# Kernel tuning notes

Hardware: AMD Instinct MI355X
Metric: run time of the kernel (lower is better)

The kernel has to match this reference:

```python
import jax, jax.numpy as jnp
import numpy as np

B, S, IN, H, K, V, OUT = 16, 200, 128, 128, 10, 50000, 10000
TW, DW = 1.0, 1.0  # time_window, dist_window


def setup_inputs() -> dict:
    key = jax.random.key(0)
    ks = jax.random.split(key, 12)
    full_seq = jax.random.randint(ks[0], (B, S), 0, V)
    length = jax.random.randint(ks[1], (B,), 1, S + 1)
    timestamp = jnp.sort(jax.random.uniform(ks[2], (B, S)), axis=1)  # sorted -> causal time_delta >= 0
    lat = jax.random.uniform(ks[3], (B, S))
    lng = jax.random.uniform(ks[4], (B, S))
    embed_table = jax.random.normal(ks[5], (V, IN)) * 0.05
    time_weights = jax.random.normal(ks[6], (K + 1, IN, H)) * (1.0 / np.sqrt(IN))
    dist_weights = jax.random.normal(ks[7], (K + 1, IN, H)) * (1.0 / np.sqrt(IN))
    hidden_weights = jax.random.normal(ks[8], (H, H)) * (1.0 / np.sqrt(H))
    W1 = jax.random.normal(ks[9], (H, 4 * H)) * 0.05
    b1 = jnp.zeros((4 * H,))
    W2 = jax.random.normal(ks[10], (4 * H, OUT)) * 0.05
    b2 = jnp.zeros((OUT,))
    return dict(full_seq=full_seq, length=length, timestamp=timestamp, lat=lat, lng=lng,
                embed_table=embed_table, time_weights=time_weights, dist_weights=dist_weights,
                hidden_weights=hidden_weights, W1=W1, b1=b1, W2=W2, b2=b2)


def reference(full_seq, length, timestamp, lat, lng, embed_table, time_weights,
              dist_weights, hidden_weights, W1, b1, W2, b2):
    x = embed_table[full_seq]                                   # [B,S,IN] (embed_layer)
    # pairwise time delta and context mask (valid target + causal j<=i + time window)
    td = timestamp[:, :, None] - timestamp[:, None, :]          # [B,S(i),S(j)]
    valid_j = length[:, None] > jnp.arange(S)[None, :]          # [B,S(j)]
    tri = jnp.arange(S)[:, None] >= jnp.arange(S)[None, :]      # i >= j (per-step slicing)
    mask = (td <= TW) & (td >= 0) & valid_j[:, None, :] & tri[None]
    # pairwise euclidean distance on (lat,lng)
    latlng = jnp.stack([lat, lng], axis=-1)                     # [B,S,2]
    dist = jnp.sqrt(((latlng[:, :, None] - latlng[:, None]) ** 2).sum(-1))
    t_idx = jnp.floor(jnp.clip(td, 0.0, TW) / TW * K).astype(jnp.int32)    # [B,S,S] in [0,K]
    d_idx = jnp.floor(jnp.clip(dist, 0.0, DW) / DW * K).astype(jnp.int32)
    # project each token x[b,j] through every slot's weight once, then gather per (i,j) bucket
    # (identical math to gathering W[t_idx] then x @ W, but avoids [B,S,S,IN,H])
    proj_t = jnp.einsum('bji,kio->bjko', x, time_weights)       # [B,S,K+1,H]
    proj_d = jnp.einsum('bji,kio->bjko', x, dist_weights)
    bI = jnp.arange(B)[:, None, None]
    jI = jnp.arange(S)[None, None, :]
    cand = 0.5 * proj_d[bI, jI, d_idx] + 0.5 * proj_t[bI, jI, t_idx]       # [B,S,S,H]
    X = jnp.where(mask[..., None], cand, 0.0).sum(2)            # [B,S,H] masked sum over context j
    # sequential sigmoid recurrence: h_i = sigmoid(X_i + h_{i-1} @ Wh)
    def step(h, xt):
        h = jax.nn.sigmoid(xt + h @ hidden_weights)
        return h, h
    _, outs = jax.lax.scan(step, jnp.zeros((B, H), X.dtype), X.transpose(1, 0, 2))
    rnn_out = outs.transpose(1, 0, 2)                           # [B,S,H]
    h_pre = rnn_out[jnp.arange(B), length - 1]                  # [B,H]
    # out_linear (dropout in eval mode = identity)
    return jnp.tanh(h_pre @ W1 + b1) @ W2 + b2                  # [B,OUT]
```

## Files before the change

kernel.cpp:

```cpp
#include <hip/hip_runtime.h>
#include <hip/hip_bf16.h>
#include <math.h>

#define B 16
#define S 200
#define IN 128
#define H 128
#define NK 11
#define OUTN 10000
#define H4 512

__global__ __launch_bounds__(512) void k_proj(
        const int* __restrict__ seq, const float* __restrict__ table,
        const int* __restrict__ length,
        const float* __restrict__ tw, const float* __restrict__ dw,
        float* __restrict__ pt, float* __restrict__ pd) {
    __shared__ float xs[32][68];
    __shared__ float wsm[32][128];
    __shared__ int sneed;
    int tid = threadIdx.x;
    int r0blk = blockIdx.x * 64;
    if (tid == 0) sneed = 0;
    __syncthreads();
    if (tid < 64) {
        int r = r0blk + tid;
        int bb = r / S, ii = r - bb * S;
        if (ii < length[bb]) sneed = 1;
    }
    __syncthreads();
    if (!sneed) return;

    int which = blockIdx.y / NK;
    int kb = blockIdx.y % NK;
    const float* W = (which == 0 ? tw : dw) + kb * IN * H;
    float* P = (which == 0 ? pt : pd);
    int tr = tid >> 5;
    int tc = tid & 31;
    int rr0 = tr * 4;

    float acc[4][4] = {{0.f}};
    for (int kk = 0; kk < IN; kk += 32) {
        {
            int r = tid >> 3;
            int kq = (tid & 7) * 4;
            int sv = seq[r0blk + r];
            float4 v = *reinterpret_cast<const float4*>(&table[sv * IN + kk + kq]);
            xs[kq + 0][r] = v.x; xs[kq + 1][r] = v.y;
            xs[kq + 2][r] = v.z; xs[kq + 3][r] = v.w;
        }
        #pragma unroll
        for (int i = 0; i < 2; ++i) {
            int f = tid + i * 512;
            int k = f >> 5; int c4 = f & 31;
            *reinterpret_cast<float4*>(&wsm[k][c4 * 4]) =
                *reinterpret_cast<const float4*>(&W[(kk + k) * H + c4 * 4]);
        }
        __syncthreads();
        #pragma unroll
        for (int k = 0; k < 32; ++k) {
            float4 a = *reinterpret_cast<const float4*>(&xs[k][rr0]);
            float4 w = *reinterpret_cast<const float4*>(&wsm[k][tc * 4]);
            acc[0][0] += a.x * w.x; acc[0][1] += a.x * w.y; acc[0][2] += a.x * w.z; acc[0][3] += a.x * w.w;
            acc[1][0] += a.y * w.x; acc[1][1] += a.y * w.y; acc[1][2] += a.y * w.z; acc[1][3] += a.y * w.w;
            acc[2][0] += a.z * w.x; acc[2][1] += a.z * w.y; acc[2][2] += a.z * w.z; acc[2][3] += a.z * w.w;
            acc[3][0] += a.w * w.x; acc[3][1] += a.w * w.y; acc[3][2] += a.w * w.z; acc[3][3] += a.w * w.w;
        }
        __syncthreads();
    }
    #pragma unroll
    for (int i = 0; i < 4; ++i) {
        int r = r0blk + rr0 + i;
        float4 v = make_float4(acc[i][0], acc[i][1], acc[i][2], acc[i][3]);
        *reinterpret_cast<float4*>(&P[(r * NK + kb) * H + tc * 4]) = v;
    }
}

__global__ __launch_bounds__(512) void k_xsum(const float* __restrict__ pt, const float* __restrict__ pd,
                       const int* __restrict__ length, const float* __restrict__ ts,
                       const float* __restrict__ lat, const float* __restrict__ lng,
                       float* __restrict__ X) {
    int wg = blockIdx.x;
    int idx = wg >> 3;
    int b = (wg & 7) + 8 * (idx / S);
    int i = idx % S;
    int len = length[b];
    if (i >= len) return;
    __shared__ float sts[S], sla[S], sln[S];
    __shared__ float psum[16][128];
    int tid = threadIdx.x;
    int jg = tid >> 5, c = tid & 31;
    if (tid < S) {
        sts[tid] = ts[b * S + tid]; sla[tid] = lat[b * S + tid]; sln[tid] = lng[b * S + tid];
    }
    __syncthreads();
    float ti = sts[i], lai = sla[i], lni = sln[i];
    float4 at = make_float4(0.f, 0.f, 0.f, 0.f);
    float4 ad = make_float4(0.f, 0.f, 0.f, 0.f);
    const float* ptb = pt + (b * S) * NK * H;
    const float* pdb = pd + (b * S) * NK * H;
    for (int j = jg; j <= i; j += 16) {
        float td = ti - sts[j];
        if (td < 0.f || td > 1.f) continue;
        int tk = (int)(td * 10.f); if (tk > 10) tk = 10;
        float dx = lai - sla[j], dy = lni - sln[j];
        float dist = sqrtf(dx * dx + dy * dy);
        int dk = (int)(dist * 10.f); if (dk > 10) dk = 10;
        float4 vt = *((const float4*)&ptb[(j * NK + tk) * H] + c);
        float4 vd = *((const float4*)&pdb[(j * NK + dk) * H] + c);
        at.x += vt.x; at.y += vt.y; at.z += vt.z; at.w += vt.w;
        ad.x += vd.x; ad.y += vd.y; ad.z += vd.z; ad.w += vd.w;
    }
    float4 s4 = make_float4(at.x + ad.x, at.y + ad.y, at.z + ad.z, at.w + ad.w);
    *reinterpret_cast<float4*>(&psum[jg][c * 4]) = s4;
    __syncthreads();
    if (tid < H) {
        float s = 0.f;
        #pragma unroll
        for (int g = 0; g < 16; ++g) s += psum[g][tid];
        X[(b * S + i) * H + tid] = 0.5f * s;
    }
}

__global__ __launch_bounds__(512) void k_rnn(const float* __restrict__ X,
        const float* __restrict__ Wh, const int* __restrict__ length,
        const float* __restrict__ W1, const float* __restrict__ b1,
        float* __restrict__ t1) {
    __shared__ float xlds[S * H];
    __shared__ float hbuf[2][H];
    int b = blockIdx.x;
    int len = length[b];
    int tid = threadIdx.x;
    int w8 = tid >> 6;
    int lane = tid & 63;
    int oo = lane >> 2;
    int kg = lane & 3;
    int o = w8 * 16 + oo;
    float wreg[32];
    #pragma unroll
    for (int it = 0; it < 8; ++it) {
        int kk = kg * 32 + ((it ^ kg) & 7) * 4;
        #pragma unroll
        for (int q = 0; q < 4; ++q)
            wreg[it * 4 + q] = Wh[(kk + q) * H + o];
    }
    {
        const float4* Xb4 = reinterpret_cast<const float4*>(X + b * S * H);
        float4* xl4 = reinterpret_cast<float4*>(xlds);
        for (int idx = tid; idx < S * H / 4; idx += 512) xl4[idx] = Xb4[idx];
    }
    if (tid < H) hbuf[0][tid] = 0.f;
    __syncthreads();
    int cur = 0;
    for (int i = 0; i < len; ++i) {
        float xc = xlds[i * H + o];
        const float* hb = &hbuf[cur][kg * 32];
        float p0 = 0.f, p1 = 0.f, p2 = 0.f, p3 = 0.f;
        #pragma unroll
        for (int it = 0; it < 8; ++it) {
            float4 hv = *reinterpret_cast<const float4*>(&hb[((it ^ kg) & 7) * 4]);
            p0 += hv.x * wreg[it * 4 + 0];
            p1 += hv.y * wreg[it * 4 + 1];
            p2 += hv.z * wreg[it * 4 + 2];
            p3 += hv.w * wreg[it * 4 + 3];
        }
        float p = (p0 + p1) + (p2 + p3);
        p += __shfl_xor(p, 1);
        p += __shfl_xor(p, 2);
        if (kg == 0) {
            float hn = 1.f / (1.f + __expf(-(xc + p)));
            hbuf[cur ^ 1][o] = hn;
        }
        __syncthreads();
        cur ^= 1;
    }
    const float* hfin = hbuf[cur];
    float acc = b1[tid];
    #pragma unroll 4
    for (int k = 0; k < H; ++k) acc += hfin[k] * W1[k * H4 + tid];
    t1[b * H4 + tid] = tanhf(acc);
}

__global__ __launch_bounds__(256) void k_fc2(const float* __restrict__ t1,
        const float* __restrict__ W2, const float* __restrict__ b2,
        float* __restrict__ out) {
    __shared__ float tls[H4 * B];
    int tid = threadIdx.x;
    int o = blockIdx.x * 64 + (tid & 63);
    int bq = tid >> 6;
    for (int idx = tid; idx < H4 * B; idx += 256) {
        int k = idx >> 4, bb = idx & 15;
        tls[idx] = t1[bb * H4 + k];
    }
    __syncthreads();
    if (o >= OUTN) return;
    float a0 = 0.f, a1 = 0.f, a2 = 0.f, a3 = 0.f;
    for (int k = 0; k < H4; ++k) {
        float wv = W2[k * OUTN + o];
        const float* tk = &tls[k * 16 + bq * 4];
        a0 += wv * tk[0]; a1 += wv * tk[1]; a2 += wv * tk[2]; a3 += wv * tk[3];
    }
    float bb2 = b2[o];
    out[(bq * 4 + 0) * OUTN + o] = a0 + bb2;
    out[(bq * 4 + 1) * OUTN + o] = a1 + bb2;
    out[(bq * 4 + 2) * OUTN + o] = a2 + bb2;
    out[(bq * 4 + 3) * OUTN + o] = a3 + bb2;
}

extern "C" void kernel_launch(void* const* d_in, const int* in_sizes, int n_in,
                              void* d_out, int out_size, void* d_ws, size_t ws_size,
                              hipStream_t stream) {
    const int*   seq    = (const int*)d_in[0];
    const int*   length = (const int*)d_in[1];
    const float* ts     = (const float*)d_in[2];
    const float* lat    = (const float*)d_in[3];
    const float* lng    = (const float*)d_in[4];
    const float* table  = (const float*)d_in[5];
    const float* tw     = (const float*)d_in[6];
    const float* dw     = (const float*)d_in[7];
    const float* wh     = (const float*)d_in[8];
    const float* W1     = (const float*)d_in[9];
    const float* b1     = (const float*)d_in[10];
    const float* W2     = (const float*)d_in[11];
    const float* b2     = (const float*)d_in[12];
    float* out = (float*)d_out;

    float* wsf  = (float*)d_ws;
    float* pt   = wsf;
    float* pd   = pt + B * S * NK * H;
    float* X    = pd + B * S * NK * H;
    float* t1   = X  + B * S * H;

    k_proj<<<dim3((B * S) / 64, 2 * NK), 512, 0, stream>>>(seq, table, length, tw, dw, pt, pd);
    k_xsum<<<B * S, 512, 0, stream>>>(pt, pd, length, ts, lat, lng, X);
    k_rnn<<<B, 512, 0, stream>>>(X, wh, length, W1, b1, t1);
    k_fc2<<<(OUTN + 63) / 64, 256, 0, stream>>>(t1, W2, b2, out);
}
```

Baseline: 249.2 us.

## Shrink RNN block to two waves with four outputs per thread

The recurrent kernel now runs with 128 threads (two wavefronts) instead of 512. Each thread holds 128 weights in registers and computes partial dot products for four output neurons. The per-step barrier therefore synchronises only two waves, which should cut the latency of the serial 200-step recurrence. In exchange, each thread does four times the FMAs per step and needs much higher register pressure. The tail W1 projection is also reworked so each thread computes four outputs.

Result: slower. 301.7 us (+21.1%).

```diff
diff --git a/kernel.cpp b/kernel.cpp
--- a/kernel.cpp
+++ b/kernel.cpp
@@ -121,7 +121,7 @@
     }
 }
 
-__global__ __launch_bounds__(512) void k_rnn(const float* __restrict__ X,
+__global__ __launch_bounds__(128) void k_rnn(const float* __restrict__ X,
         const float* __restrict__ Wh, const int* __restrict__ length,
         const float* __restrict__ W1, const float* __restrict__ b1,
         float* __restrict__ t1) {
@@ -130,54 +130,68 @@
     int b = blockIdx.x;
     int len = length[b];
     int tid = threadIdx.x;
-    int w8 = tid >> 6;
     int lane = tid & 63;
-    int oo = lane >> 2;
+    int wv = tid >> 6;
+    int og = wv * 16 + (lane >> 2);
     int kg = lane & 3;
-    int o = w8 * 16 + oo;
-    float wreg[32];
+    int o0 = og * 4;
+    float4 w4[8][4];
     #pragma unroll
     for (int it = 0; it < 8; ++it) {
-        int kk = kg * 32 + ((it ^ kg) & 7) * 4;
-        #pragma unroll
-        for (int q = 0; q < 4; ++q)
-            wreg[it * 4 + q] = Wh[(kk + q) * H + o];
+        int k0 = kg * 32 + ((it ^ kg) & 7) * 4;
+        #pragma unroll
+        for (int q = 0; q < 4; ++q) {
+            w4[it][q].x = Wh[(k0 + 0) * H + o0 + q];
+            w4[it][q].y = Wh[(k0 + 1) * H + o0 + q];
+            w4[it][q].z = Wh[(k0 + 2) * H + o0 + q];
+            w4[it][q].w = Wh[(k0 + 3) * H + o0 + q];
+        }
     }
     {
         const float4* Xb4 = reinterpret_cast<const float4*>(X + b * S * H);
         float4* xl4 = reinterpret_cast<float4*>(xlds);
-        for (int idx = tid; idx < S * H / 4; idx += 512) xl4[idx] = Xb4[idx];
+        for (int idx = tid; idx < S * H / 4; idx += 128) xl4[idx] = Xb4[idx];
     }
     if (tid < H) hbuf[0][tid] = 0.f;
     __syncthreads();
     int cur = 0;
     for (int i = 0; i < len; ++i) {
-        float xc = xlds[i * H + o];
         const float* hb = &hbuf[cur][kg * 32];
-        float p0 = 0.f, p1 = 0.f, p2 = 0.f, p3 = 0.f;
+        float4 a0 = make_float4(0.f,0.f,0.f,0.f), a1 = a0, a2 = a0, a3 = a0;
         #pragma unroll
         for (int it = 0; it < 8; ++it) {
             float4 hv = *reinterpret_cast<const float4*>(&hb[((it ^ kg) & 7) * 4]);
-            p0 += hv.x * wreg[it * 4 + 0];
-            p1 += hv.y * wreg[it * 4 + 1];
-            p2 += hv.z * wreg[it * 4 + 2];
-            p3 += hv.w * wreg[it * 4 + 3];
-        }
-        float p = (p0 + p1) + (p2 + p3);
-        p += __shfl_xor(p, 1);
-        p += __shfl_xor(p, 2);
-        if (kg == 0) {
-            float hn = 1.f / (1.f + __expf(-(xc + p)));
-            hbuf[cur ^ 1][o] = hn;
-        }
+            a0.x += hv.x * w4[it][0].x; a0.y += hv.y * w4[it][0].y; a0.z += hv.z * w4[it][0].z; a0.w += hv.w * w4[it][0].w;
+            a1.x += hv.x * w4[it][1].x; a1.y += hv.y * w4[it][1].y; a1.z += hv.z * w4[it][1].z; a1.w += hv.w * w4[it][1].w;
+            a2.x += hv.x * w4[it][2].x; a2.y += hv.y * w4[it][2].y; a2.z += hv.z * w4[it][2].z; a2.w += hv.w * w4[it][2].w;
+            a3.x += hv.x * w4[it][3].x; a3.y += hv.y * w4[it][3].y; a3.z += hv.z * w4[it][3].z; a3.w += hv.w * w4[it][3].w;
+        }
+        float p0 = (a0.x + a0.y) + (a0.z + a0.w);
+        float p1 = (a1.x + a1.y) + (a1.z + a1.w);
+        float p2 = (a2.x + a2.y) + (a2.z + a2.w);
+        float p3 = (a3.x + a3.y) + (a3.z + a3.w);
+        p0 += __shfl_xor(p0, 1); p0 += __shfl_xor(p0, 2);
+        p1 += __shfl_xor(p1, 1); p1 += __shfl_xor(p1, 2);
+        p2 += __shfl_xor(p2, 1); p2 += __shfl_xor(p2, 2);
+        p3 += __shfl_xor(p3, 1); p3 += __shfl_xor(p3, 2);
+        float p = (kg == 0) ? p0 : (kg == 1) ? p1 : (kg == 2) ? p2 : p3;
+        float xc = xlds[i * H + o0 + kg];
+        float hn = 1.f / (1.f + __expf(-(xc + p)));
+        hbuf[cur ^ 1][o0 + kg] = hn;
         __syncthreads();
         cur ^= 1;
     }
     const float* hfin = hbuf[cur];
-    float acc = b1[tid];
-    #pragma unroll 4
-    for (int k = 0; k < H; ++k) acc += hfin[k] * W1[k * H4 + tid];
-    t1[b * H4 + tid] = tanhf(acc);
+    float c0 = b1[tid], c1 = b1[tid + 128], c2 = b1[tid + 256], c3 = b1[tid + 384];
+    for (int k = 0; k < H; ++k) {
+        float hv = hfin[k];
+        const float* wr = &W1[k * H4 + tid];
+        c0 += hv * wr[0]; c1 += hv * wr[128]; c2 += hv * wr[256]; c3 += hv * wr[384];
+    }
+    t1[b * H4 + tid]       = tanhf(c0);
+    t1[b * H4 + tid + 128] = tanhf(c1);
+    t1[b * H4 + tid + 256] = tanhf(c2);
+    t1[b * H4 + tid + 384] = tanhf(c3);
 }
 
 __global__ __launch_bounds__(256) void k_fc2(const float* __restrict__ t1,
@@ -232,6 +246,6 @@
 
     k_proj<<<dim3((B * S) / 64, 2 * NK), 512, 0, stream>>>(seq, table, length, tw, dw, pt, pd);
     k_xsum<<<B * S, 512, 0, stream>>>(pt, pd, length, ts, lat, lng, X);
-    k_rnn<<<B, 512, 0, stream>>>(X, wh, length, W1, b1, t1);
+    k_rnn<<<B, 128, 0, stream>>>(X, wh, length, W1, b1, t1);
     k_fc2<<<(OUTN + 63) / 64, 256, 0, stream>>>(t1, W2, b2, out);
 }
```
